# Performance work log

Hardware: AMD Instinct MI355X
Metric: run time of the kernel (lower is better)

The kernel has to match this reference:

```python
import jax, jax.numpy as jnp
import numpy as np

B, D, T, H, C = 65536, 1024, 16, 128, 10


def setup_inputs() -> dict:
    key = jax.random.key(0)
    k1, k2, k3, k4, k5, k6 = jax.random.split(key, 6)
    x = jax.random.normal(k1, (B, D), dtype=jnp.float32)
    task_id = jax.random.randint(k2, (B,), 0, T, dtype=jnp.int32)
    # per-task head params (torch nn.Linear init scale ~ 1/sqrt(fan_in))
    W1 = jax.random.normal(k3, (T, D, H), dtype=jnp.float32) / np.sqrt(D)
    b1 = jax.random.normal(k4, (T, H), dtype=jnp.float32) * 0.01
    W2 = jax.random.normal(k5, (T, H, C), dtype=jnp.float32) / np.sqrt(H)
    b2 = jax.random.normal(k6, (T, C), dtype=jnp.float32) * 0.01
    return {"x": x, "task_id": task_id, "W1": W1, "b1": b1, "W2": W2, "b2": b2}


def reference(x, task_id, W1, b1, W2, b2):
    # Dense dispatch: run every head on every sample as one big GEMM
    # (x @ [T*H] concatenated weights), then select each sample's task head.
    # Same math as the torch per-task mask/gather/scatter loop (eval mode,
    # dropout is identity).
    h = jax.nn.relu(jnp.einsum('bd,tdh->bth', x, W1) + b1)      # [B,T,H]
    logits_all = jnp.einsum('bth,thc->btc', h, W2) + b2          # [B,T,C]
    # gather the row for each sample's task_id
    logits = jnp.take_along_axis(
        logits_all, task_id[:, None, None].astype(jnp.int32), axis=1
    ).squeeze(1)                                                 # [B,C]
    return logits
```

## Files before the change

kernel.cpp:

```cpp
#include <hip/hip_runtime.h>
#include <hip/hip_bf16.h>

#define TASKS 16
#define DIM 1024
#define HID 128
#define NCLS 10
#define NB 65536
#define BM 128
#define NTILES (NB / BM + TASKS)

#define WS_TOT  4096
#define WS_RIDX 4160
#define WS_W1S  (WS_RIDX + NB)

typedef __attribute__((ext_vector_type(8))) short bf16x8;
typedef __attribute__((ext_vector_type(4))) float f32x4;
typedef __attribute__((ext_vector_type(2))) unsigned u32x2;

__device__ __forceinline__ unsigned short f2bf(float f) {
    union { __hip_bfloat16 h; unsigned short s; } u; u.h = __float2bfloat16(f); return u.s;
}

__device__ __forceinline__ void glds16(const void* gsrc, void* ldst) {
    __builtin_amdgcn_global_load_lds(
        (const __attribute__((address_space(1))) unsigned*)gsrc,
        (__attribute__((address_space(3))) unsigned*)ldst, 16, 0, 0);
}

__global__ __launch_bounds__(256) void k_pre(const int* __restrict__ tid_arr,
                                             const float* __restrict__ W1,
                                             const float* __restrict__ W2,
                                             int* __restrict__ ws) {
    const int blk = blockIdx.x, tid = threadIdx.x;
    if (blk < 256) {
        __shared__ int l[TASKS];
        if (tid < TASKS) l[tid] = 0;
        __syncthreads();
        atomicAdd(&l[tid_arr[blk * 256 + tid]], 1);
        __syncthreads();
        if (tid < TASKS) ws[blk * TASKS + tid] = l[tid];
    } else if (blk < 768) {
        const int idx = blk - 256;
        const int t = idx >> 5, kt = idx & 31;
        __shared__ float ld[32 * 132];
        const float* src = W1 + ((size_t)t * DIM + kt * 32) * HID;
        #pragma unroll
        for (int r = 0; r < 16; ++r) {
            const int fl = r * 256 + tid;
            ld[(fl >> 7) * 132 + (fl & 127)] = src[fl];
        }
        __syncthreads();
        char* dst = (char*)((short*)(ws + WS_W1S) + ((size_t)(t * 32 + kt) << 12));
        const int col = tid >> 1, half = tid & 1;
        #pragma unroll
        for (int g = 0; g < 2; ++g) {
            const int lgk = (half * 2 + g) ^ (col & 3);
            bf16x8 v;
            #pragma unroll
            for (int j = 0; j < 8; ++j)
                v[j] = (short)f2bf(ld[(lgk * 8 + j) * 132 + col]);
            *(bf16x8*)(dst + tid * 32 + g * 16) = v;
        }
    } else {
        const int t = blk - 768;
        short* W2t = (short*)(ws + WS_W1S) + ((size_t)TASKS * 32 * 4096);
        #pragma unroll
        for (int i = 0; i < 8; ++i) {
            const int o = i * 256 + tid, c = o >> 7, h = o & 127;
            const float v = (c < NCLS) ? W2[((size_t)t * HID + h) * NCLS + c] : 0.f;
            W2t[((size_t)t * 16 + c) * HID + h] = (short)f2bf(v);
        }
    }
}

__global__ __launch_bounds__(256) void k_scatter(const int* __restrict__ tid_arr,
                                                 int* __restrict__ ws) {
    __shared__ int part[256 * TASKS];
    __shared__ int l[TASKS], offl[TASKS], prel[TASKS];
    const int b = blockIdx.x, tid = threadIdx.x;
    #pragma unroll
    for (int r = 0; r < 16; ++r) part[r * 256 + tid] = ws[r * 256 + tid];
    if (tid < TASKS) l[tid] = 0;
    __syncthreads();
    const int i = b * 256 + tid;
    const int t = tid_arr[i];
    const int rank = atomicAdd(&l[t], 1);
    __syncthreads();
    if (tid < TASKS) {
        int pre = 0, tot = 0;
        for (int bb = 0; bb < 256; ++bb) {
            const int v = part[bb * TASKS + tid];
            if (bb < b) pre += v;
            tot += v;
        }
        prel[tid] = pre;
        part[tid] = tot;
        if (b == 0) ws[WS_TOT + tid] = tot;
    }
    __syncthreads();
    if (tid == 0) {
        int ro = 0;
        for (int k = 0; k < TASKS; ++k) { offl[k] = ro; ro += part[k]; }
    }
    __syncthreads();
    ws[WS_RIDX + offl[t] + prel[t] + rank] = i;
}

__global__ __launch_bounds__(256, 4) void k_main(
    const float* __restrict__ x, const float* __restrict__ b1,
    const float* __restrict__ b2, const int* __restrict__ ws,
    float* __restrict__ out)
{
    __shared__ __align__(16) short smem[16384];
    __shared__ int ridx[BM];

    const int* tot = ws + WS_TOT;
    const int* rowIdx = ws + WS_RIDX;
    const short* W1s = (const short*)(ws + WS_W1S);
    const short* W2t = W1s + ((size_t)TASKS * 32 * 4096);

    const int w = (blockIdx.x & 7) * (NTILES / 8) + (blockIdx.x >> 3);

    int t = -1, m = 0, gstart = 0;
    {
        int accT = 0, accO = 0;
        for (int k = 0; k < TASKS; ++k) {
            const int c = tot[k], nt = (c + BM - 1) >> 7;
            if (t < 0 && w < accT + nt) {
                t = k; gstart = accO + (w - accT) * BM;
                m = c - (w - accT) * BM; if (m > BM) m = BM;
            }
            accT += nt; accO += c;
        }
    }
    if (t < 0) return;

    const int tid = threadIdx.x;
    if (tid < BM) ridx[tid] = rowIdx[gstart + (tid < m ? tid : m - 1)];
    __syncthreads();

    const int lane = tid & 63, wv = tid >> 6;
    const int lg = lane >> 4, lr = lane & 15;
    const int wrow = (wv >> 1) * 64, wcol = (wv & 1) * 64;

    const float* gpA[4];
    unsigned wbA[4];
    #pragma unroll
    for (int j = 0; j < 4; ++j) {
        const int row = wv * 32 + j * 8 + (lane >> 3);
        gpA[j] = x + ((size_t)ridx[row] << 10) + (lane & 7) * 4;
        wbA[j] = row * 64 + ((((lane & 7) >> 1) ^ (row & 3)) << 4) + (lane & 1) * 8;
    }
    const char* w1sT = (const char*)W1s + ((size_t)t << 18);
    const int bi = wv * 2;

    f32x4 a8[4];
    f32x4 acc[4][4] = {};
    const unsigned sw = (unsigned)((lg ^ (lr & 3)) << 4);

    auto LOADA = [&](int kt) {
        #pragma unroll
        for (int j = 0; j < 4; ++j) a8[j] = *(const f32x4*)(gpA[j] + kt * 32);
    };
    auto WRITEA = [&](int buf) {
        char* ab = (char*)smem + buf * 16384;
        #pragma unroll
        for (int j = 0; j < 4; ++j) {
            u32x2 pk;
            pk[0] = ((unsigned)f2bf(a8[j][1]) << 16) | (unsigned)f2bf(a8[j][0]);
            pk[1] = ((unsigned)f2bf(a8[j][3]) << 16) | (unsigned)f2bf(a8[j][2]);
            *(u32x2*)(ab + wbA[j]) = pk;
        }
    };
    auto ISSUEB = [&](int buf, int kt) {
        const char* src = w1sT + ((size_t)kt << 13) + bi * 1024 + lane * 16;
        char* dst = (char*)smem + buf * 16384 + 8192 + bi * 1024;
        glds16(src, dst);
        glds16(src + 1024, dst + 1024);
    };
    auto COMPUTE = [&](int buf) {
        const char* ab = (const char*)smem + buf * 16384;
        const char* bb = ab + 8192;
        bf16x8 af[4], bfr[4];
        #pragma unroll
        for (int rf = 0; rf < 4; ++rf)
            af[rf] = *(const bf16x8*)(ab + (wrow + rf * 16 + lr) * 64 + sw);
        #pragma unroll
        for (int cf = 0; cf < 4; ++cf)
            bfr[cf] = *(const bf16x8*)(bb + (wcol + cf * 16 + lr) * 64 + sw);
        #pragma unroll
        for (int rf = 0; rf < 4; ++rf)
            #pragma unroll
            for (int cf = 0; cf < 4; ++cf)
                acc[rf][cf] = __builtin_amdgcn_mfma_f32_16x16x32_bf16(af[rf], bfr[cf], acc[rf][cf], 0, 0, 0);
    };

    LOADA(0);
    ISSUEB(0, 0);
    WRITEA(0);
    LOADA(1);
    asm volatile("s_waitcnt vmcnt(4) lgkmcnt(0)" ::: "memory");
    __builtin_amdgcn_s_barrier();
    __builtin_amdgcn_sched_barrier(0);

    #pragma unroll 2
    for (int kt = 0; kt < 32; ++kt) {
        const int buf = kt & 1;
        ISSUEB(buf ^ 1, kt + 1 < 32 ? kt + 1 : 31);
        WRITEA(buf ^ 1);
        LOADA(kt + 2 < 32 ? kt + 2 : 31);
        COMPUTE(buf);
        asm volatile("s_waitcnt vmcnt(4) lgkmcnt(0)" ::: "memory");
        __builtin_amdgcn_s_barrier();
        __builtin_amdgcn_sched_barrier(0);
    }
    __syncthreads();

    short* hl = smem;
    #pragma unroll
    for (int cf = 0; cf < 4; ++cf) {
        const int col = wcol + cf * 16 + lr;
        const float b1v = b1[t * HID + col];
        #pragma unroll
        for (int rf = 0; rf < 4; ++rf)
            #pragma unroll
            for (int q = 0; q < 4; ++q) {
                const int row = wrow + rf * 16 + lg * 4 + q;
                const float hv = fmaxf(acc[rf][cf][q] + b1v, 0.f);
                *(unsigned short*)((char*)hl + row * 256 +
                    (((col >> 3) ^ (row & 7)) << 4) + (col & 7) * 2) = f2bf(hv);
            }
    }
    __syncthreads();

    f32x4 acc2[2] = {};
    #pragma unroll
    for (int ks = 0; ks < 4; ++ks) {
        bf16x8 bvv = *(const bf16x8*)(W2t + (((size_t)t * 16 + lr) << 7) + ks * 32 + lg * 8);
        #pragma unroll
        for (int rf = 0; rf < 2; ++rf) {
            const int row = wv * 32 + rf * 16 + lr;
            bf16x8 avv = *(const bf16x8*)((const char*)hl + row * 256 +
                             (((ks * 4 + lg) ^ (row & 7)) << 4));
            acc2[rf] = __builtin_amdgcn_mfma_f32_16x16x32_bf16(avv, bvv, acc2[rf], 0, 0, 0);
        }
    }
    if (lr < NCLS) {
        const float b2v = b2[t * NCLS + lr];
        #pragma unroll
        for (int rf = 0; rf < 2; ++rf)
            #pragma unroll
            for (int q = 0; q < 4; ++q) {
                const int row = wv * 32 + rf * 16 + lg * 4 + q;
                if (row < m) out[(size_t)ridx[row] * NCLS + lr] = acc2[rf][q] + b2v;
            }
    }
}

extern "C" void kernel_launch(void* const* d_in, const int* in_sizes, int n_in,
                              void* d_out, int out_size, void* d_ws, size_t ws_size,
                              hipStream_t stream) {
    (void)in_sizes; (void)n_in; (void)out_size; (void)ws_size;
    const float* x       = (const float*)d_in[0];
    const int*   task_id = (const int*)d_in[1];
    const float* W1      = (const float*)d_in[2];
    const float* b1      = (const float*)d_in[3];
    const float* W2      = (const float*)d_in[4];
    const float* b2      = (const float*)d_in[5];
    float* out = (float*)d_out;
    int* ws = (int*)d_ws;
    k_pre<<<784, 256, 0, stream>>>(task_id, W1, W2, ws);
    k_scatter<<<256, 256, 0, stream>>>(task_id, ws);
    k_main<<<NTILES, 256, 0, stream>>>(x, b1, b2, ws, out);
}
```

Before: 82.80 us.

## Fuse pre, scatter and main into one cooperative kernel with grid syncs

Merges the three launches (histogram/weight conversion, scatter, grouped GEMM) into a single cooperative kernel separated by grid-wide syncs, which removes inter-kernel launch gaps. The scatter prefix sum is also restructured into a two-level sum over 16-block chunks instead of a serial 256-iteration loop per task. The multi-kernel path is kept as a fallback if the cooperative launch fails. The trade-off is the cost of the grid syncs and the need for the whole grid (528 blocks) to be co-resident.

New measurement: 219.8 us. 165% more time.

```diff
diff --git a/kernel.cpp b/kernel.cpp
--- a/kernel.cpp
+++ b/kernel.cpp
@@ -1,5 +1,8 @@
 #include <hip/hip_runtime.h>
 #include <hip/hip_bf16.h>
+#include <hip/hip_cooperative_groups.h>
+
+namespace cg = cooperative_groups;
 
 #define TASKS 16
 #define DIM 1024
@@ -27,99 +30,97 @@
         (__attribute__((address_space(3))) unsigned*)ldst, 16, 0, 0);
 }
 
-__global__ __launch_bounds__(256) void k_pre(const int* __restrict__ tid_arr,
-                                             const float* __restrict__ W1,
-                                             const float* __restrict__ W2,
-                                             int* __restrict__ ws) {
-    const int blk = blockIdx.x, tid = threadIdx.x;
-    if (blk < 256) {
-        __shared__ int l[TASKS];
-        if (tid < TASKS) l[tid] = 0;
-        __syncthreads();
-        atomicAdd(&l[tid_arr[blk * 256 + tid]], 1);
-        __syncthreads();
-        if (tid < TASKS) ws[blk * TASKS + tid] = l[tid];
-    } else if (blk < 768) {
-        const int idx = blk - 256;
-        const int t = idx >> 5, kt = idx & 31;
-        __shared__ float ld[32 * 132];
-        const float* src = W1 + ((size_t)t * DIM + kt * 32) * HID;
-        #pragma unroll
-        for (int r = 0; r < 16; ++r) {
-            const int fl = r * 256 + tid;
-            ld[(fl >> 7) * 132 + (fl & 127)] = src[fl];
-        }
-        __syncthreads();
-        char* dst = (char*)((short*)(ws + WS_W1S) + ((size_t)(t * 32 + kt) << 12));
-        const int col = tid >> 1, half = tid & 1;
-        #pragma unroll
-        for (int g = 0; g < 2; ++g) {
-            const int lgk = (half * 2 + g) ^ (col & 3);
-            bf16x8 v;
-            #pragma unroll
-            for (int j = 0; j < 8; ++j)
-                v[j] = (short)f2bf(ld[(lgk * 8 + j) * 132 + col]);
-            *(bf16x8*)(dst + tid * 32 + g * 16) = v;
-        }
-    } else {
-        const int t = blk - 768;
-        short* W2t = (short*)(ws + WS_W1S) + ((size_t)TASKS * 32 * 4096);
-        #pragma unroll
-        for (int i = 0; i < 8; ++i) {
-            const int o = i * 256 + tid, c = o >> 7, h = o & 127;
-            const float v = (c < NCLS) ? W2[((size_t)t * HID + h) * NCLS + c] : 0.f;
-            W2t[((size_t)t * 16 + c) * HID + h] = (short)f2bf(v);
-        }
-    }
-}
-
-__global__ __launch_bounds__(256) void k_scatter(const int* __restrict__ tid_arr,
-                                                 int* __restrict__ ws) {
-    __shared__ int part[256 * TASKS];
-    __shared__ int l[TASKS], offl[TASKS], prel[TASKS];
-    const int b = blockIdx.x, tid = threadIdx.x;
+
+__device__ __forceinline__ void phase_hist(const int* tid_arr, int* ws, int blk,
+                                           int tid, int* l) {
+    if (tid < TASKS) l[tid] = 0;
+    __syncthreads();
+    atomicAdd(&l[tid_arr[blk * 256 + tid]], 1);
+    __syncthreads();
+    if (tid < TASKS) ws[blk * TASKS + tid] = l[tid];
+}
+
+__device__ __forceinline__ void phase_w1(const float* W1, int* ws, int unit,
+                                         int tid, float* ld ) {
+    const int t = unit >> 5, kt = unit & 31;
+    const float* src = W1 + ((size_t)t * DIM + kt * 32) * HID;
+    #pragma unroll
+    for (int r = 0; r < 16; ++r) {
+        const int fl = r * 256 + tid;
+        ld[(fl >> 7) * 132 + (fl & 127)] = src[fl];
+    }
+    __syncthreads();
+    char* dst = (char*)((short*)(ws + WS_W1S) + ((size_t)(t * 32 + kt) << 12));
+    const int col = tid >> 1, half = tid & 1;
+    #pragma unroll
+    for (int g = 0; g < 2; ++g) {
+        const int lgk = (half * 2 + g) ^ (col & 3);
+        bf16x8 v;
+        #pragma unroll
+        for (int j = 0; j < 8; ++j)
+            v[j] = (short)f2bf(ld[(lgk * 8 + j) * 132 + col]);
+        *(bf16x8*)(dst + tid * 32 + g * 16) = v;
+    }
+}
+
+__device__ __forceinline__ void phase_w2(const float* W2, int* ws, int t, int tid) {
+    short* W2t = (short*)(ws + WS_W1S) + ((size_t)TASKS * 32 * 4096);
+    #pragma unroll
+    for (int i = 0; i < 8; ++i) {
+        const int o = i * 256 + tid, c = o >> 7, h = o & 127;
+        const float v = (c < NCLS) ? W2[((size_t)t * HID + h) * NCLS + c] : 0.f;
+        W2t[((size_t)t * 16 + c) * HID + h] = (short)f2bf(v);
+    }
+}
+
+__device__ __forceinline__ void phase_scatter(const int* tid_arr, int* ws, int b,
+                                              int tid, int* part, int* sums,
+                                              int* l, int* offl, int* prel, int* totl) {
     #pragma unroll
     for (int r = 0; r < 16; ++r) part[r * 256 + tid] = ws[r * 256 + tid];
     if (tid < TASKS) l[tid] = 0;
     __syncthreads();
-    const int i = b * 256 + tid;
-    const int t = tid_arr[i];
+    const int t = tid_arr[b * 256 + tid];
     const int rank = atomicAdd(&l[t], 1);
+    {
+        const int c = tid >> 4, tt = tid & 15;
+        int s = 0;
+        #pragma unroll
+        for (int bb = 0; bb < 16; ++bb) s += part[(c * 16 + bb) * TASKS + tt];
+        sums[c * TASKS + tt] = s;
+    }
     __syncthreads();
     if (tid < TASKS) {
-        int pre = 0, tot = 0;
-        for (int bb = 0; bb < 256; ++bb) {
-            const int v = part[bb * TASKS + tid];
-            if (bb < b) pre += v;
-            tot += v;
-        }
-        prel[tid] = pre;
-        part[tid] = tot;
+        const int cb = b >> 4;
+        int pre = 0;
+        for (int c = 0; c < cb; ++c) pre += sums[c * TASKS + tid];
+        for (int bb = cb * 16; bb < b; ++bb) pre += part[bb * TASKS + tid];
+        int tot = 0;
+        #pragma unroll
+        for (int c = 0; c < 16; ++c) tot += sums[c * TASKS + tid];
+        prel[tid] = pre; totl[tid] = tot;
         if (b == 0) ws[WS_TOT + tid] = tot;
     }
     __syncthreads();
     if (tid == 0) {
         int ro = 0;
-        for (int k = 0; k < TASKS; ++k) { offl[k] = ro; ro += part[k]; }
-    }
-    __syncthreads();
-    ws[WS_RIDX + offl[t] + prel[t] + rank] = i;
-}
-
-__global__ __launch_bounds__(256, 4) void k_main(
+        for (int k = 0; k < TASKS; ++k) { offl[k] = ro; ro += totl[k]; }
+    }
+    __syncthreads();
+    ws[WS_RIDX + offl[t] + prel[t] + rank] = b * 256 + tid;
+}
+
+__device__ __forceinline__ void phase_main(
     const float* __restrict__ x, const float* __restrict__ b1,
     const float* __restrict__ b2, const int* __restrict__ ws,
-    float* __restrict__ out)
+    float* __restrict__ out, int bid, int tid, short* smem, int* ridx)
 {
-    __shared__ __align__(16) short smem[16384];
-    __shared__ int ridx[BM];
-
     const int* tot = ws + WS_TOT;
     const int* rowIdx = ws + WS_RIDX;
     const short* W1s = (const short*)(ws + WS_W1S);
     const short* W2t = W1s + ((size_t)TASKS * 32 * 4096);
 
-    const int w = (blockIdx.x & 7) * (NTILES / 8) + (blockIdx.x >> 3);
+    const int w = (bid & 7) * (NTILES / 8) + (bid >> 3);
 
     int t = -1, m = 0, gstart = 0;
     {
@@ -135,7 +136,6 @@
     }
     if (t < 0) return;
 
-    const int tid = threadIdx.x;
     if (tid < BM) ridx[tid] = rowIdx[gstart + (tid < m ? tid : m - 1)];
     __syncthreads();
 
@@ -257,6 +257,60 @@
     }
 }
 
+__global__ __launch_bounds__(256, 4) void k_all(
+    const int* __restrict__ task_id, const float* __restrict__ W1,
+    const float* __restrict__ W2, const float* __restrict__ x,
+    const float* __restrict__ b1, const float* __restrict__ b2,
+    int* __restrict__ ws, float* __restrict__ out)
+{
+    __shared__ __align__(16) char LB[33280];
+    __shared__ int l[TASKS], offl[TASKS], prel[TASKS], totl[TASKS];
+    cg::grid_group grid = cg::this_grid();
+    const int w = blockIdx.x, tid = threadIdx.x;
+
+    if (w < 256) phase_hist(task_id, ws, w, tid, l);
+    if (w < 512) phase_w1(W1, ws, w, tid, (float*)LB);
+    else         phase_w2(W2, ws, w - 512, tid);
+    grid.sync();
+
+    if (w < 256)
+        phase_scatter(task_id, ws, w, tid, (int*)LB, (int*)(LB + 16384),
+                      l, offl, prel, totl);
+    grid.sync();
+
+    phase_main(x, b1, b2, ws, out, w, tid, (short*)LB, (int*)(LB + 32768));
+}
+
+__global__ __launch_bounds__(256) void k_pre(const int* __restrict__ tid_arr,
+                                             const float* __restrict__ W1,
+                                             const float* __restrict__ W2,
+                                             int* __restrict__ ws) {
+    __shared__ __align__(16) char LB[16896];
+    __shared__ int l[TASKS];
+    const int blk = blockIdx.x, tid = threadIdx.x;
+    if (blk < 256) phase_hist(tid_arr, ws, blk, tid, l);
+    else if (blk < 768) phase_w1(W1, ws, blk - 256, tid, (float*)LB);
+    else phase_w2(W2, ws, blk - 768, tid);
+}
+
+__global__ __launch_bounds__(256) void k_scatter(const int* __restrict__ tid_arr,
+                                                 int* __restrict__ ws) {
+    __shared__ __align__(16) char LB[17408];
+    __shared__ int l[TASKS], offl[TASKS], prel[TASKS], totl[TASKS];
+    phase_scatter(tid_arr, ws, blockIdx.x, threadIdx.x,
+                  (int*)LB, (int*)(LB + 16384), l, offl, prel, totl);
+}
+
+__global__ __launch_bounds__(256, 4) void k_main(
+    const float* __restrict__ x, const float* __restrict__ b1,
+    const float* __restrict__ b2, const int* __restrict__ ws,
+    float* __restrict__ out)
+{
+    __shared__ __align__(16) char LB[33280];
+    phase_main(x, b1, b2, ws, out, blockIdx.x, threadIdx.x,
+               (short*)LB, (int*)(LB + 32768));
+}
+
 extern "C" void kernel_launch(void* const* d_in, const int* in_sizes, int n_in,
                               void* d_out, int out_size, void* d_ws, size_t ws_size,
                               hipStream_t stream) {
@@ -269,7 +323,14 @@
     const float* b2      = (const float*)d_in[5];
     float* out = (float*)d_out;
     int* ws = (int*)d_ws;
-    k_pre<<<784, 256, 0, stream>>>(task_id, W1, W2, ws);
-    k_scatter<<<256, 256, 0, stream>>>(task_id, ws);
-    k_main<<<NTILES, 256, 0, stream>>>(x, b1, b2, ws, out);
-}
+
+    void* args[] = { (void*)&task_id, (void*)&W1, (void*)&W2, (void*)&x,
+                     (void*)&b1, (void*)&b2, (void*)&ws, (void*)&out };
+    hipError_t e = hipLaunchCooperativeKernel((void*)k_all, dim3(NTILES), dim3(256),
+                                              args, 0, stream);
+    if (e != hipSuccess) {
+        k_pre<<<784, 256, 0, stream>>>(task_id, W1, W2, ws);
+        k_scatter<<<256, 256, 0, stream>>>(task_id, ws);
+        k_main<<<NTILES, 256, 0, stream>>>(x, b1, b2, ws, out);
+    }
+}
```
